# Kernel optimization log

Measured on AMD Instinct MI355X. Metric: run time of the kernel, lower is better.

The kernel has to match this reference:

```python
import jax, jax.numpy as jnp
import numpy as np
from jax import lax

B, T, V = 128, 256, 64
HF = 32   # MLP feature-imputation hidden
CTX = 32  # context hidden
HID = 64  # LSTM hidden


def _uniform(k, shape, fan):
    s = 1.0 / np.sqrt(fan)
    return jax.random.uniform(k, shape, jnp.float32, -s, s)


def setup_inputs():
    key = jax.random.key(0)
    ks = jax.random.split(key, 40)
    values = jax.random.normal(ks[0], (B, T, V), jnp.float32)
    masks = (jax.random.uniform(ks[1], (B, T, V)) > 0.3).astype(jnp.float32)
    deltas = jax.random.uniform(ks[2], (B, T, V), jnp.float32) * 5.0
    lengths = jax.random.randint(ks[3], (B,), T // 2, T + 1)
    min_vals = jnp.min(values, axis=1, keepdims=True)
    max_vals = jnp.max(values, axis=1, keepdims=True)
    D_in = 2 * V + 2 * CTX
    return dict(
        lengths=lengths, values=values, masks=masks, deltas=deltas,
        min_vals=min_vals, max_vals=max_vals,
        W_decay=_uniform(ks[4], (V, V), V), b_decay=_uniform(ks[5], (V,), V),
        W_feat=_uniform(ks[6], (V, HF, V), V), b_feat=_uniform(ks[7], (V, HF), V),
        W_nl1=_uniform(ks[8], (HF, HF), HF), b_nl1=_uniform(ks[9], (HF,), HF),
        W_nl2=_uniform(ks[10], (1, HF), HF), b_nl2=_uniform(ks[11], (1,), HF),
        Wc1=_uniform(ks[12], (2 * CTX, 3 * V + 1), 3 * V + 1), bc1=_uniform(ks[13], (2 * CTX,), 3 * V + 1),
        Wc2=_uniform(ks[14], (CTX, 2 * CTX), 2 * CTX), bc2=_uniform(ks[15], (CTX,), 2 * CTX),
        W_ih_g=_uniform(ks[16], (3 * CTX, 2 * V), CTX), W_hh_g=_uniform(ks[17], (3 * CTX, CTX), CTX),
        b_ih_g=_uniform(ks[18], (3 * CTX,), CTX), b_hh_g=_uniform(ks[19], (3 * CTX,), CTX),
        W_init=_uniform(ks[20], (2 * HID, 2 * CTX), 2 * CTX), b_init=_uniform(ks[21], (2 * HID,), 2 * CTX),
        W_ih_f=_uniform(ks[22], (4 * HID, D_in), HID), W_hh_f=_uniform(ks[23], (4 * HID, HID), HID),
        b_ih_f=_uniform(ks[24], (4 * HID,), HID), b_hh_f=_uniform(ks[25], (4 * HID,), HID),
        W_ih_b=_uniform(ks[26], (4 * HID, D_in), HID), W_hh_b=_uniform(ks[27], (4 * HID, HID), HID),
        b_ih_b=_uniform(ks[28], (4 * HID,), HID), b_hh_b=_uniform(ks[29], (4 * HID,), HID),
        W_ri=_uniform(ks[30], (V, 2 * HID), 2 * HID), b_ri=_uniform(ks[31], (V,), 2 * HID),
        W_fu=_uniform(ks[32], (V, 2 * V), 2 * V), b_fu=_uniform(ks[33], (V,), 2 * V),
    )


def _gru(x, h, Wih, Whh, bih, bhh):
    gi = x @ Wih.T + bih
    gh = h @ Whh.T + bhh
    ir, iz, inn = jnp.split(gi, 3, axis=-1)
    hr, hz, hn = jnp.split(gh, 3, axis=-1)
    r = jax.nn.sigmoid(ir + hr)
    z = jax.nn.sigmoid(iz + hz)
    n = jnp.tanh(inn + r * hn)
    return (1.0 - z) * n + z * h


def _lstm(x, h, c, Wih, Whh, bih, bhh):
    g = x @ Wih.T + bih + h @ Whh.T + bhh
    i, f, gg, o = jnp.split(g, 4, axis=-1)
    c = jax.nn.sigmoid(f) * c + jax.nn.sigmoid(i) * jnp.tanh(gg)
    h = jax.nn.sigmoid(o) * jnp.tanh(c)
    return h, c


def _forward(lengths, values, masks, deltas, min_vals, max_vals,
             W_decay, b_decay, W_feat, b_feat, W_nl1, b_nl1, W_nl2, b_nl2,
             Wc1, bc1, Wc2, bc2, W_ih_g, W_hh_g, b_ih_g, b_hh_g,
             W_init, b_init, W_ih_f, W_hh_f, b_ih_f, b_hh_f,
             W_ih_b, W_hh_b, b_ih_b, b_hh_b, W_ri, b_ri, W_fu, b_fu):
    Bb, Tt, Vv = values.shape
    lf = lengths.astype(jnp.float32)
    pad = (jnp.arange(Tt)[None, :] + 1 <= lengths[:, None]).astype(jnp.float32)  # [B,T]

    msum = masks.sum(axis=1)                       # [B,V] observation counts
    means = values.sum(axis=1) / msum
    var = ((values - means[:, None, :]) ** 2).sum(axis=1) / (msum - 1.0)
    stdev = jnp.sqrt(var)
    missing = 1.0 - msum / lf[:, None]
    stats = jnp.concatenate([lf[:, None], means, stdev, missing], axis=1)  # [B,3V+1]

    mmn = jnp.maximum(max_vals - min_vals, 1e-8)   # [B,1,V]
    nv = (values - min_vals) / mmn
    nmeans = (means - min_vals[:, 0, :]) / mmn[:, 0, :]

    # last-observation-carried-forward x_prime
    nv_tm = jnp.swapaxes(nv, 0, 1)   # [T,B,V]
    m_tm = jnp.swapaxes(masks, 0, 1)

    def pstep(xp, xm):
        x_prev, m_prev = xm
        xp = m_prev * x_prev + (1.0 - m_prev) * xp
        return xp, xp
    _, xp_rest = lax.scan(pstep, nv_tm[0], (nv_tm[:-1], m_tm[:-1]))
    x_prime = jnp.swapaxes(jnp.concatenate([nv_tm[:1], xp_rest], axis=0), 0, 1)

    # InputTemporalDecay: F.linear(d, W*I, b) == d * diag(W) + b
    gamma = jnp.exp(-jax.nn.relu(deltas * jnp.diag(W_decay) + b_decay))
    x_decay = gamma * x_prime + (1.0 - gamma) * nmeans[:, None, :]
    x_complete = masks * nv + (1.0 - masks) * x_decay

    # context vectors
    ctx_mlp = jax.nn.relu(stats @ Wc1.T + bc1) @ Wc2.T + bc2  # [B,CTX]
    x_rnn_tm = jnp.swapaxes(jnp.concatenate([x_complete, masks], axis=-1), 0, 1)  # [T,B,2V]
    pad_tm = jnp.swapaxes(pad, 0, 1)[:, :, None]
    h0 = jnp.zeros((Bb, W_hh_g.shape[1]), values.dtype)

    def gstep(carry, inp):
        h, hn = carry
        x_t, p_t = inp
        h = _gru(x_t, h, W_ih_g, W_hh_g, b_ih_g, b_hh_g)
        hn = p_t * h + (1.0 - p_t) * hn
        return (h, hn), None
    (_, ctx_rnn), _ = lax.scan(gstep, (h0, h0), (x_rnn_tm, pad_tm))
    context = jnp.concatenate([ctx_mlp, ctx_rnn], axis=1)  # [B,2*CTX]

    hinit = context @ W_init.T + b_init  # [B,2H]
    cinit = jnp.tanh(hinit)
    Hh = hinit.shape[1] // 2
    hf0, hb0 = hinit[:, :Hh], hinit[:, Hh:]
    cf0, cb0 = cinit[:, :Hh], cinit[:, Hh:]

    ctx_bt = jnp.broadcast_to(context[:, None, :], (Bb, Tt, context.shape[1]))
    rnn_in_tm = jnp.swapaxes(jnp.concatenate([x_complete, masks, ctx_bt], axis=-1), 0, 1)  # [T,B,D]

    def fstep(carry, x):
        h, c = _lstm(x, carry[0], carry[1], W_ih_f, W_hh_f, b_ih_f, b_hh_f)
        return (h, c), h
    _, hf_rest = lax.scan(fstep, (hf0, cf0), rnn_in_tm[:-1])
    hf_all = jnp.concatenate([hf0[None], hf_rest], axis=0)  # [T,B,H]

    def bstep(carry, x):
        h, c = _lstm(x, carry[0], carry[1], W_ih_b, W_hh_b, b_ih_b, b_hh_b)
        return (h, c), h
    _, hb_rest = lax.scan(bstep, (hb0, cb0), rnn_in_tm[1:][::-1])  # t = T-1 .. 1
    hb_all = jnp.concatenate([hb0[None], hb_rest], axis=0)[::-1]   # time-aligned

    h_cat = jnp.concatenate([hf_all, hb_all], axis=-1)  # [T,B,2H]
    rnn_imp = jnp.swapaxes(h_cat @ W_ri.T + b_ri, 0, 1)  # [B,T,V]

    # per-variable masked feature imputation (no self-connection)
    eye = jnp.eye(Vv, dtype=values.dtype)
    Wm = W_feat * (1.0 - eye[:, None, :])                 # [V,HF,V]
    hidden = jnp.einsum('btv,ghv->btgh', x_complete, Wm) + b_feat  # [B,T,V,HF]
    z = jax.nn.relu(hidden) @ W_nl1.T + b_nl1
    feat_imp = (jax.nn.relu(z) @ W_nl2.T + b_nl2)[..., 0]  # [B,T,V]

    beta = jax.nn.sigmoid(jnp.concatenate([gamma, masks], axis=-1) @ W_fu.T + b_fu)
    final_imp = beta * feat_imp + (1.0 - beta) * rnn_imp

    # unnormalize all three estimates; stack as [3,B,T,V]
    out = jnp.stack([rnn_imp, feat_imp, final_imp], axis=0) * mmn[None] + min_vals[None]
    return out


def reference(lengths, values, masks, deltas, min_vals, max_vals,
              W_decay, b_decay, W_feat, b_feat, W_nl1, b_nl1, W_nl2, b_nl2,
              Wc1, bc1, Wc2, bc2, W_ih_g, W_hh_g, b_ih_g, b_hh_g,
              W_init, b_init, W_ih_f, W_hh_f, b_ih_f, b_hh_f,
              W_ih_b, W_hh_b, b_ih_b, b_hh_b, W_ri, b_ri, W_fu, b_fu):
    return _forward(lengths, values, masks, deltas, min_vals, max_vals,
                    W_decay, b_decay, W_feat, b_feat, W_nl1, b_nl1, W_nl2, b_nl2,
                    Wc1, bc1, Wc2, bc2, W_ih_g, W_hh_g, b_ih_g, b_hh_g,
                    W_init, b_init, W_ih_f, W_hh_f, b_ih_f, b_hh_f,
                    W_ih_b, W_hh_b, b_ih_b, b_hh_b, W_ri, b_ri, W_fu, b_fu)
```

## Files before the change

kernel.cpp:

```cpp
#include <hip/hip_runtime.h>
#include <hip/hip_fp16.h>

static constexpr int NB = 128;
static constexpr int NT = 256;
static constexpr int NV = 64;
static constexpr int NBT = NB * NT;
static constexpr int NBTV = NBT * NV;

typedef __attribute__((ext_vector_type(8))) short short8;
typedef __attribute__((ext_vector_type(4))) float f32x4;
typedef __attribute__((ext_vector_type(4))) float fvec4;

__device__ __forceinline__ void wave_lds_fence() {
    __builtin_amdgcn_sched_barrier(0);
    asm volatile("s_waitcnt lgkmcnt(0)" ::: "memory");
    __builtin_amdgcn_sched_barrier(0);
}

__device__ __forceinline__ void block_sync_lds() {
    __builtin_amdgcn_sched_barrier(0);
    asm volatile("s_waitcnt lgkmcnt(0)" ::: "memory");
    __builtin_amdgcn_s_barrier();
    asm volatile("" ::: "memory");
    __builtin_amdgcn_sched_barrier(0);
}

__device__ __forceinline__ unsigned short f2bf(float x) {
    unsigned int u = __float_as_uint(x);
    return (unsigned short)((u + 0x7FFFu + ((u >> 16) & 1u)) >> 16);
}
__device__ __forceinline__ float bf2f(unsigned short b) {
    return __uint_as_float(((unsigned int)b) << 16);
}
__device__ __forceinline__ unsigned short f2h(float x) {
    union { _Float16 h; unsigned short u; } c; c.h = (_Float16)x; return c.u;
}
__device__ __forceinline__ float fsigm(float x) {
    return __builtin_amdgcn_rcpf(1.0f + __expf(-x));
}
__device__ __forceinline__ float ftanh(float x) {
    return 1.0f - 2.0f * __builtin_amdgcn_rcpf(1.0f + __expf(2.0f * x));
}

__device__ __forceinline__ short8 pack8(float4 a, float4 b) {
    short8 r;
    r[0] = (short)f2bf(a.x); r[1] = (short)f2bf(a.y); r[2] = (short)f2bf(a.z); r[3] = (short)f2bf(a.w);
    r[4] = (short)f2bf(b.x); r[5] = (short)f2bf(b.y); r[6] = (short)f2bf(b.z); r[7] = (short)f2bf(b.w);
    return r;
}

__device__ __forceinline__ void dot4(float4& acc, const float4 wv, const float4 xv) {
    acc.x = fmaf(wv.x, xv.x, acc.x);
    acc.y = fmaf(wv.y, xv.y, acc.y);
    acc.z = fmaf(wv.z, xv.z, acc.z);
    acc.w = fmaf(wv.w, xv.w, acc.w);
}

__global__ __launch_bounds__(256) void k_prep(
    const float* __restrict__ Wf, const float* __restrict__ Wihf,
    const float* __restrict__ Wihb, const float* __restrict__ Wihg,
    const float* __restrict__ Whhf, const float* __restrict__ Whhb,
    const float* __restrict__ Whhg, const float* __restrict__ Wri,
    const float* __restrict__ Wfu,
    unsigned short* __restrict__ wbf, float* __restrict__ wdiag,
    unsigned short* __restrict__ wgf, unsigned short* __restrict__ wgb,
    unsigned short* __restrict__ wgg,
    unsigned short* __restrict__ whhf_h, unsigned short* __restrict__ whhb_h,
    unsigned short* __restrict__ whhg_h,
    unsigned short* __restrict__ wri_bf, unsigned short* __restrict__ wfu_bf) {
    int i = blockIdx.x * 256 + threadIdx.x;
    if (i < NV * 32 * NV) wbf[i] = f2bf(Wf[i]);
    if (i < 2048) wdiag[i] = bf2f(f2bf(Wf[i * 64 + (i >> 5)]));
    if (i < 32768) {
        int n = i >> 7, k = i & 127;
        wgf[i] = f2bf(Wihf[n * 192 + k]);
        wgb[i] = f2bf(Wihb[n * 192 + k]);
    }
    if (i < 12288) wgg[i] = f2bf(Wihg[i]);
    if (i < 16384) { whhf_h[i] = f2h(Whhf[i]); whhb_h[i] = f2h(Whhb[i]); }
    if (i < 3072) whhg_h[i] = f2h(Whhg[i]);
    if (i < 8192) { wri_bf[i] = f2bf(Wri[i]); wfu_bf[i] = f2bf(Wfu[i]); }
}

__global__ __launch_bounds__(256) void k_fill(
    const int* __restrict__ lengths,
    const float* __restrict__ values, const float* __restrict__ masks,
    const float* __restrict__ deltas, const float* __restrict__ minv,
    const float* __restrict__ maxv,
    const float* __restrict__ Wd, const float* __restrict__ bd,
    float* __restrict__ stats,
    float* __restrict__ mmn_ws, float* __restrict__ nmeans_ws,
    float* __restrict__ xcomp, unsigned short* __restrict__ gam,
    const unsigned short* __restrict__ wgg, const float* __restrict__ bihg,
    float* __restrict__ gg) {
    int b = blockIdx.x; int tid = threadIdx.x;
    int v = tid & 63; int tc = tid >> 6;
    float mn = minv[b * NV + v];
    size_t base = (size_t)b * NT * NV + v;
    __shared__ float red[3][4][64];
    __shared__ float lastv[4][64];
    __shared__ int hasf[4][64];
    __shared__ float nv0s[64];
    __shared__ float smm[64], snm[64];
    __shared__ __align__(16) unsigned short sxc[256][64];
    int t0 = tc * 64;
    float sv = 0.f, sq = 0.f, sm = 0.f;
    float last = 0.f; int has = 0;
    for (int t = t0; t < t0 + 64; t++) {
        float val = values[base + (size_t)t * NV];
        float m = masks[base + (size_t)t * NV];
        sv += val; sq += val * val; sm += m;
        if (m != 0.f) { last = val; has = 1; }
        if (tc == 0 && t == 0) nv0s[v] = val;
    }
    red[0][tc][v] = sv; red[1][tc][v] = sq; red[2][tc][v] = sm;
    lastv[tc][v] = last; hasf[tc][v] = has;
    __syncthreads();
    if (tc == 0) {
        sv = red[0][0][v] + red[0][1][v] + red[0][2][v] + red[0][3][v];
        sq = red[1][0][v] + red[1][1][v] + red[1][2][v] + red[1][3][v];
        sm = red[2][0][v] + red[2][1][v] + red[2][2][v] + red[2][3][v];
        float mean = sv / sm;
        float var = (sq - 2.0f * mean * sv + (float)NT * mean * mean) / (sm - 1.0f);
        var = fmaxf(var, 0.0f);
        float sd = sqrtf(var);
        float lf = (float)lengths[b];
        float miss = 1.0f - sm / lf;
        float mx = maxv[b * NV + v];
        float mm = fmaxf(mx - mn, 1e-8f);
        float* st = stats + b * 256;
        if (v == 0) st[0] = lf;
        st[1 + v] = mean; st[65 + v] = sd; st[129 + v] = miss;
        float nmean = (mean - mn) / mm;
        mmn_ws[b * NV + v] = mm;
        nmeans_ws[b * NV + v] = nmean;
        smm[v] = mm; snm[v] = nmean;
    }
    __syncthreads();
    float mm = smm[v];
    float nmean = snm[v];
    float wd = Wd[v * NV + v], bdv = bd[v];
    float xp = (nv0s[v] - mn) / mm;
    for (int q = tc - 1; q >= 0; q--) {
        if (hasf[q][v]) { xp = (lastv[q][v] - mn) / mm; break; }
    }
    for (int t = t0; t < t0 + 64; t++) {
        size_t i = base + (size_t)t * NV;
        float val = values[i], m = masks[i], d = deltas[i];
        float nv = (val - mn) / mm;
        float g = expf(-fmaxf(fmaf(d, wd, bdv), 0.0f));
        float xd = g * xp + (1.0f - g) * nmean;
        float xc = m * nv + (1.0f - m) * xd;
        xcomp[i] = xc; gam[i] = f2bf(g);
        sxc[t][v] = f2bf(xc);
        xp = (m != 0.f) ? nv : xp;
    }
    __syncthreads();
    int lane = tid & 63;
    int r = lane & 15, kc = lane >> 4;
    for (int tile = 0; tile < 4; tile++) {
        int trow = (tc * 4 + tile) * 16;
        int bt0 = b * NT + trow;
        short8 af0 = *(const short8*)&sxc[trow + r][kc * 8];
        short8 af1 = *(const short8*)&sxc[trow + r][32 + kc * 8];
        const float* mr = masks + ((size_t)bt0 + r) * NV + kc * 8;
        short8 af2 = pack8(*(const float4*)(mr), *(const float4*)(mr + 4));
        short8 af3 = pack8(*(const float4*)(mr + 32), *(const float4*)(mr + 36));
        #pragma unroll 3
        for (int nt = 0; nt < 6; nt++) {
            const unsigned short* w = wgg + (size_t)(nt * 16 + r) * 128 + kc * 8;
            float bias = bihg[nt * 16 + r];
            f32x4 acc = {bias, bias, bias, bias};
            acc = __builtin_amdgcn_mfma_f32_16x16x32_bf16(af0, *(const short8*)(w), acc, 0, 0, 0);
            acc = __builtin_amdgcn_mfma_f32_16x16x32_bf16(af1, *(const short8*)(w + 32), acc, 0, 0, 0);
            acc = __builtin_amdgcn_mfma_f32_16x16x32_bf16(af2, *(const short8*)(w + 64), acc, 0, 0, 0);
            acc = __builtin_amdgcn_mfma_f32_16x16x32_bf16(af3, *(const short8*)(w + 96), acc, 0, 0, 0);
            #pragma unroll
            for (int i = 0; i < 4; i++)
                gg[(size_t)(bt0 + kc * 4 + i) * 96 + nt * 16 + r] = acc[i];
        }
    }
}

#define GRU_STEP(T, GIN) { \
    const int t_ = (T); const int p_ = t_ & 1; \
    int4 raw_[4]; \
    const int4* hp_ = (const int4*)hsg[g][s]; \
    _Pragma("unroll") for (int q = 0; q < 4; q++) raw_[q] = hp_[q]; \
    const __half2* hhv_ = (const __half2*)raw_; \
    __half2 a0_ = zh2, a1_ = zh2, a2_ = zh2, a3_ = zh2; \
    _Pragma("unroll") for (int q = 0; q < 16; q += 4) { \
        a0_ = __hfma2(w2[q],     hhv_[q],     a0_); \
        a1_ = __hfma2(w2[q + 1], hhv_[q + 1], a1_); \
        a2_ = __hfma2(w2[q + 2], hhv_[q + 2], a2_); \
        a3_ = __hfma2(w2[q + 3], hhv_[q + 3], a3_); } \
    __half2 sA_ = __hadd2(__hadd2(a0_, a1_), __hadd2(a2_, a3_)); \
    float d_ = __low2float(sA_) + __high2float(sA_); \
    if (g < 2) { \
        gexg[p_][s][n][g] = GIN + bh + d_; \
    } else { \
        gexg[p_][s][n][2] = bh + d_; \
        gexg[p_][s][n][3] = GIN; \
    } \
    block_sync_lds(); \
    float qx_ = gexg[p_][s][n][0], qy_ = gexg[p_][s][n][1]; \
    float qz_ = gexg[p_][s][n][2], qw_ = gexg[p_][s][n][3]; \
    float rr_ = fsigm(qx_); \
    float zz_ = fsigm(qy_); \
    float nn_ = ftanh(qw_ + rr_ * qz_); \
    float h_ = (1.f - zz_) * nn_ + zz_ * hprev; \
    hprev = h_; \
    if (t_ < len) hn = h_; \
    hsg[g][s][n] = f2h(h_); \
    wave_lds_fence(); \
}

#define FEAT_BODY(BT0) { \
    int bt0 = (BT0); \
    int r = lane & 15, kc = lane >> 4; \
    unsigned short* hbw = hbs[wave]; \
    float* lx = ldsx[wave]; \
    float* flw = fls[wave]; \
    short8 a0, a1; \
    { \
        const float* xr = xcomp + (size_t)(bt0 + r) * NV + kc * 8; \
        a0 = pack8(*(const float4*)(xr), *(const float4*)(xr + 4)); \
        a1 = pack8(*(const float4*)(xr + 32), *(const float4*)(xr + 36)); \
    } \
    { \
        int gc0 = kc * 16; \
        const float* xr2 = xcomp + (size_t)(bt0 + r) * NV + gc0; \
        _Pragma("unroll") for (int e = 0; e < 16; e += 4) { \
            float4 p = *(const float4*)(xr2 + e); \
            lx[(gc0 + e + 0) * 16 + r] = bf2f(f2bf(p.x)); \
            lx[(gc0 + e + 1) * 16 + r] = bf2f(f2bf(p.y)); \
            lx[(gc0 + e + 2) * 16 + r] = bf2f(f2bf(p.z)); \
            lx[(gc0 + e + 3) * 16 + r] = bf2f(f2bf(p.w)); \
        } \
    } \
    short8 wb0, wb1; \
    { \
        const float* w = Wnl1 + r * 32 + kc * 8; \
        wb0 = pack8(*(const float4*)w, *(const float4*)(w + 4)); \
        const float* w2p = Wnl1 + (16 + r) * 32 + kc * 8; \
        wb1 = pack8(*(const float4*)w2p, *(const float4*)(w2p + 4)); \
    } \
    float b0i[4], b1i[4], w2a[4], w2b[4]; \
    _Pragma("unroll") for (int i = 0; i < 4; i++) { \
        b0i[i] = bnl1[kc * 4 + i]; \
        b1i[i] = bnl1[16 + kc * 4 + i]; \
        w2a[i] = Wnl2[kc * 4 + i]; \
        w2b[i] = Wnl2[16 + kc * 4 + i]; \
    } \
    float bn2 = bnl2[0]; \
    __builtin_amdgcn_wave_barrier(); \
    _Pragma("unroll 2") for (int g = 0; g < 64; g++) { \
        __builtin_amdgcn_wave_barrier(); \
        float xv[4]; \
        _Pragma("unroll") for (int i = 0; i < 4; i++) xv[i] = lx[g * 16 + kc * 4 + i]; \
        _Pragma("unroll") for (int f = 0; f < 2; f++) { \
            int n0 = g * 32 + f * 16; \
            const unsigned short* wrow = wbf + (size_t)(n0 + r) * 64; \
            short8 b0 = *(const short8*)(wrow + kc * 8); \
            short8 b1 = *(const short8*)(wrow + 32 + kc * 8); \
            f32x4 acc = {0.f, 0.f, 0.f, 0.f}; \
            acc = __builtin_amdgcn_mfma_f32_16x16x32_bf16(a0, b0, acc, 0, 0, 0); \
            acc = __builtin_amdgcn_mfma_f32_16x16x32_bf16(a1, b1, acc, 0, 0, 0); \
            int n = n0 + r; \
            float wd = wdiag[n], bs = bfeat[n]; \
            _Pragma("unroll") for (int i = 0; i < 4; i++) { \
                float h = acc[i] - xv[i] * wd + bs; \
                h = fmaxf(h, 0.0f); \
                hbw[(kc * 4 + i) * 32 + f * 16 + r] = f2bf(h); \
            } \
        } \
        __builtin_amdgcn_wave_barrier(); \
        short8 ah = *(const short8*)(hbw + r * 32 + kc * 8); \
        f32x4 zt0 = {0.f, 0.f, 0.f, 0.f}, zt1 = {0.f, 0.f, 0.f, 0.f}; \
        zt0 = __builtin_amdgcn_mfma_f32_16x16x32_bf16(wb0, ah, zt0, 0, 0, 0); \
        zt1 = __builtin_amdgcn_mfma_f32_16x16x32_bf16(wb1, ah, zt1, 0, 0, 0); \
        float p = 0.f; \
        _Pragma("unroll") for (int i = 0; i < 4; i++) { \
            p = fmaf(fmaxf(zt0[i] + b0i[i], 0.0f), w2a[i], p); \
            p = fmaf(fmaxf(zt1[i] + b1i[i], 0.0f), w2b[i], p); \
        } \
        p += __shfl_xor(p, 16, 64); \
        p += __shfl_xor(p, 32, 64); \
        if (lane < 16) flw[lane * 65 + g] = p + bn2; \
    } \
    __builtin_amdgcn_wave_barrier(); \
    _Pragma("unroll") for (int q = 0; q < 16; q++) \
        feat_out[(size_t)(bt0 + q) * NV + lane] = flw[q * 65 + lane]; \
}

__global__ __launch_bounds__(256, 1) void k_mid(
    const float* __restrict__ gg_t, const int* __restrict__ lengths,
    const unsigned short* __restrict__ whhg_h, const float* __restrict__ bhh,
    float* __restrict__ ctx,
    const float* __restrict__ stats, const float* __restrict__ Wc1,
    const float* __restrict__ bc1, const float* __restrict__ Wc2,
    const float* __restrict__ bc2,
    const float* __restrict__ xcomp, const float* __restrict__ masks,
    const unsigned short* __restrict__ wbf,
    const float* __restrict__ wdiag, const float* __restrict__ bfeat,
    const float* __restrict__ Wnl1, const float* __restrict__ bnl1,
    const float* __restrict__ Wnl2, const float* __restrict__ bnl2,
    float* __restrict__ feat_out,
    const unsigned short* __restrict__ wgf, const unsigned short* __restrict__ wgb,
    float* __restrict__ gf, float* __restrict__ gb) {
    __shared__ __align__(16) unsigned short hsg[3][2][32];
    __shared__ __align__(16) float gexg[2][2][32][5];
    __shared__ __align__(16) float ss[193];
    __shared__ float h1[64];
    __shared__ __align__(16) unsigned short hbs[4][16 * 32];
    __shared__ __align__(16) float ldsx[4][64 * 16];
    __shared__ __align__(16) float fls[4][16 * 65];

    int bx = blockIdx.x;
    int tid = threadIdx.x;

    if (bx < 64) {
        int b0 = bx * 2;
        int g = tid >> 6;
        int lane = tid & 63;
        int s = lane >> 5, n = lane & 31;
        if (g == 3) {
            for (int t = 0; t < NT; t++) block_sync_lds();
            return;
        }
        int b = b0 + s;
        const __half2 zh2 = __float2half2_rn(0.f);
        int4 w4[4];
        {
            const int4* wp = (const int4*)(whhg_h + (size_t)(g * 32 + n) * 32);
            #pragma unroll
            for (int q = 0; q < 4; q++) w4[q] = wp[q];
        }
        const __half2* w2 = (const __half2*)w4;
        float bh = bhh[g * 32 + n];
        int len = lengths[b];
        float hprev = 0.f, hn = 0.f;
        hsg[g][s][n] = f2h(0.f);
        const float* gbase = gg_t + (size_t)b * NT * 96;
        #define GGIDX(T) ((size_t)(T) * 96 + g * 32 + n)
        float gi0 = gbase[GGIDX(0)];
        float gi1 = gbase[GGIDX(1)];
        float gi2 = gbase[GGIDX(2)];
        float gi3 = gbase[GGIDX(3)];
        wave_lds_fence();
        for (int t = 0; t < 252; t += 4) {
            GRU_STEP(t, gi0)
            gi0 = gbase[GGIDX(t + 4)];
            GRU_STEP(t + 1, gi1)
            gi1 = gbase[GGIDX(t + 5)];
            GRU_STEP(t + 2, gi2)
            gi2 = gbase[GGIDX(t + 6)];
            GRU_STEP(t + 3, gi3)
            gi3 = gbase[GGIDX(t + 7)];
        }
        GRU_STEP(252, gi0)
        GRU_STEP(253, gi1)
        GRU_STEP(254, gi2)
        GRU_STEP(255, gi3)
        #undef GGIDX
        if (g == 0) ctx[(b0 + s) * 64 + 32 + n] = hn;
    } else if (bx < 192) {
        if (tid >= 64) return;
        int b = bx - 64;
        ss[tid] = stats[b * 256 + tid];
        ss[64 + tid] = stats[b * 256 + 64 + tid];
        ss[128 + tid] = stats[b * 256 + 128 + tid];
        if (tid == 0) ss[192] = stats[b * 256 + 192];
        wave_lds_fence();
        float acc = bc1[tid];
        const float* w = Wc1 + (size_t)tid * 193;
        for (int k = 0; k < 193; k++) acc = fmaf(w[k], ss[k], acc);
        h1[tid] = fmaxf(acc, 0.f);
        wave_lds_fence();
        if (tid < 32) {
            float a = bc2[tid];
            const float* w2 = Wc2 + tid * 64;
            for (int k = 0; k < 64; k++) a = fmaf(w2[k], h1[k], a);
            ctx[b * 64 + tid] = a;
        }
    } else if (bx < 448) {
        int wave = tid >> 6; int lane = tid & 63;
        FEAT_BODY((bx - 192) * 64 + wave * 16)
    } else {
        int wave = tid >> 6, lane = tid & 63;
        int bt0 = (bx - 448) * 64 + wave * 16;
        int r = lane & 15, kc = lane >> 4;
        const float* xr = xcomp + (size_t)(bt0 + r) * NV + kc * 8;
        const float* mr = masks + (size_t)(bt0 + r) * NV + kc * 8;
        short8 af0 = pack8(*(const float4*)(xr), *(const float4*)(xr + 4));
        short8 af1 = pack8(*(const float4*)(xr + 32), *(const float4*)(xr + 36));
        short8 af2 = pack8(*(const float4*)(mr), *(const float4*)(mr + 4));
        short8 af3 = pack8(*(const float4*)(mr + 32), *(const float4*)(mr + 36));
        #pragma unroll 4
        for (int nt = 0; nt < 16; nt++) {
            const unsigned short* w = wgf + (size_t)(nt * 16 + r) * 128 + kc * 8;
            f32x4 acc = {0.f, 0.f, 0.f, 0.f};
            acc = __builtin_amdgcn_mfma_f32_16x16x32_bf16(af0, *(const short8*)(w), acc, 0, 0, 0);
            acc = __builtin_amdgcn_mfma_f32_16x16x32_bf16(af1, *(const short8*)(w + 32), acc, 0, 0, 0);
            acc = __builtin_amdgcn_mfma_f32_16x16x32_bf16(af2, *(const short8*)(w + 64), acc, 0, 0, 0);
            acc = __builtin_amdgcn_mfma_f32_16x16x32_bf16(af3, *(const short8*)(w + 96), acc, 0, 0, 0);
            int col = nt * 16 + r, g = col >> 6, n = col & 63;
            #pragma unroll
            for (int i = 0; i < 4; i++)
                gf[((size_t)(bt0 + kc * 4 + i) * 64 + n) * 4 + g] = acc[i];
        }
        #pragma unroll 4
        for (int nt = 0; nt < 16; nt++) {
            const unsigned short* w = wgb + (size_t)(nt * 16 + r) * 128 + kc * 8;
            f32x4 acc = {0.f, 0.f, 0.f, 0.f};
            acc = __builtin_amdgcn_mfma_f32_16x16x32_bf16(af0, *(const short8*)(w), acc, 0, 0, 0);
            acc = __builtin_amdgcn_mfma_f32_16x16x32_bf16(af1, *(const short8*)(w + 32), acc, 0, 0, 0);
            acc = __builtin_amdgcn_mfma_f32_16x16x32_bf16(af2, *(const short8*)(w + 64), acc, 0, 0, 0);
            acc = __builtin_amdgcn_mfma_f32_16x16x32_bf16(af3, *(const short8*)(w + 96), acc, 0, 0, 0);
            int col = nt * 16 + r, g = col >> 6, n = col & 63;
            #pragma unroll
            for (int i = 0; i < 4; i++)
                gb[((size_t)(bt0 + kc * 4 + i) * 64 + n) * 4 + g] = acc[i];
        }
    }
}

#define LSTM_STEP(S, GIN) { \
    const int s_ = (S); const int p_ = s_ & 1; \
    int4 raw_[8]; \
    const int4* hp_ = (const int4*)hs[g]; \
    _Pragma("unroll") for (int q = 0; q < 8; q++) raw_[q] = hp_[q]; \
    const __half2* hhv_ = (const __half2*)raw_; \
    __half2 a0_ = zh2, a1_ = zh2, a2_ = zh2, a3_ = zh2; \
    _Pragma("unroll") for (int q = 0; q < 32; q += 4) { \
        a0_ = __hfma2(w2[q],     hhv_[q],     a0_); \
        a1_ = __hfma2(w2[q + 1], hhv_[q + 1], a1_); \
        a2_ = __hfma2(w2[q + 2], hhv_[q + 2], a2_); \
        a3_ = __hfma2(w2[q + 3], hhv_[q + 3], a3_); } \
    __half2 sA_ = __hadd2(__hadd2(a0_, a1_), __hadd2(a2_, a3_)); \
    float d_ = __low2float(sA_) + __high2float(sA_); \
    gex[p_][n][g] = GIN + ctg + d_; \
    block_sync_lds(); \
    float qx_ = gex[p_][n][0], qy_ = gex[p_][n][1]; \
    float qz_ = gex[p_][n][2], qw_ = gex[p_][n][3]; \
    float ii_ = fsigm(qx_); \
    float ff_ = fsigm(qy_); \
    float gv_ = ftanh(qz_); \
    float oo_ = fsigm(qw_); \
    c = ff_ * c + ii_ * gv_; \
    float hv_ = oo_ * ftanh(c); \
    if (g == 0) { \
        int tout_ = dir ? (NT - 2 - s_) : (s_ + 1); \
        hall[((size_t)b * NT + tout_) * NV + n] = hv_; \
    } \
    hs[g][n] = f2h(hv_); \
    wave_lds_fence(); \
}

__global__ __launch_bounds__(256, 1) void k_lstm(
    const float* __restrict__ gf, const float* __restrict__ gb,
    const float* __restrict__ ctx,
    const unsigned short* __restrict__ whhf_h, const unsigned short* __restrict__ whhb_h,
    const float* __restrict__ Wihf, const float* __restrict__ Wihb,
    const float* __restrict__ bihf, const float* __restrict__ bhhf,
    const float* __restrict__ bihb, const float* __restrict__ bhhb,
    const float* __restrict__ Wini, const float* __restrict__ bini,
    float* __restrict__ out0, float* __restrict__ out1,
    const float* __restrict__ xcomp, const unsigned short* __restrict__ wbf,
    const float* __restrict__ wdiag, const float* __restrict__ bfeat,
    const float* __restrict__ Wnl1, const float* __restrict__ bnl1,
    const float* __restrict__ Wnl2, const float* __restrict__ bnl2,
    float* __restrict__ feat_out) {
    __shared__ __align__(16) unsigned short hs[4][64];
    __shared__ __align__(16) float gex[2][64][5];
    __shared__ __align__(16) float sctx[64];
    __shared__ __align__(16) float sh0[64];
    __shared__ __align__(16) unsigned short hbs[4][16 * 32];
    __shared__ __align__(16) float ldsx[4][64 * 16];
    __shared__ __align__(16) float fls[4][16 * 65];

    int bx = blockIdx.x;
    int tid = threadIdx.x;

    if (bx >= 256) {
        int wave = tid >> 6; int lane = tid & 63;
        FEAT_BODY((bx - 256) * 64 + 16384 + wave * 16)
        return;
    }

    int dir = bx >> 7; int b = bx & 127;
    int g = tid >> 6;
    int n = tid & 63;
    const float* gates = dir ? gb : gf;
    const unsigned short* wsrc = dir ? whhb_h : whhf_h;
    float* hall = dir ? out1 : out0;
    const __half2 zh2 = __float2half2_rn(0.f);
    int4 w4[8];
    {
        const int4* wp = (const int4*)(wsrc + (size_t)(g * 64 + n) * 64);
        #pragma unroll
        for (int q = 0; q < 8; q++) w4[q] = wp[q];
    }
    const __half2* w2 = (const __half2*)w4;
    size_t gbase = (size_t)b * NT * 256;
    #define GIDX(S) (gbase + (size_t)(dir ? (NT - 1 - (S)) : (S)) * 256 + n * 4 + g)
    float gi0 = gates[GIDX(0)];
    float gi1 = gates[GIDX(1)];
    float gi2 = gates[GIDX(2)];
    float gi3 = gates[GIDX(3)];
    if (tid < 64) sctx[tid] = ctx[b * 64 + tid];
    __syncthreads();
    float ctg;
    {
        const float4* wc = (const float4*)((dir ? Wihb : Wihf) + (size_t)tid * 192 + 128);
        float bias = dir ? (bihb[tid] + bhhb[tid]) : (bihf[tid] + bhhf[tid]);
        const float4* c4 = (const float4*)sctx;
        float4 a = {0, 0, 0, 0};
        #pragma unroll
        for (int q = 0; q < 16; q++) dot4(a, wc[q], c4[q]);
        ctg = bias + a.x + a.y + a.z + a.w;
    }
    if (tid < 64) {
        const float4* wi = (const float4*)(Wini + (size_t)(dir * 64 + tid) * 64);
        const float4* c4 = (const float4*)sctx;
        float4 a = {0, 0, 0, 0};
        #pragma unroll
        for (int q = 0; q < 16; q++) dot4(a, wi[q], c4[q]);
        sh0[tid] = bini[dir * 64 + tid] + a.x + a.y + a.z + a.w;
    }
    __syncthreads();
    float c;
    {
        float h0 = sh0[n];
        c = ftanh(h0);
        hs[g][n] = f2h(h0);
        if (g == 0) {
            int t0 = dir ? (NT - 1) : 0;
            hall[((size_t)b * NT + t0) * NV + n] = h0;
        }
    }
    wave_lds_fence();
    for (int sx = 0; sx < 252; sx += 4) {
        LSTM_STEP(sx, gi0)
        gi0 = gates[GIDX(sx + 4)];
        LSTM_STEP(sx + 1, gi1)
        gi1 = gates[GIDX(sx + 5)];
        LSTM_STEP(sx + 2, gi2)
        gi2 = gates[GIDX(sx + 6)];
        LSTM_STEP(sx + 3, gi3)
        gi3 = gates[GIDX(sx + 7)];
    }
    LSTM_STEP(252, gi0)
    LSTM_STEP(253, gi1)
    LSTM_STEP(254, gi2)
    #undef GIDX
}

__global__ __launch_bounds__(256) void k_post(
    const unsigned short* __restrict__ gam, const float* __restrict__ masks,
    const unsigned short* __restrict__ wri_bf, const unsigned short* __restrict__ wfu_bf,
    const float* __restrict__ bri, const float* __restrict__ bfu,
    const float* __restrict__ mmn_ws, const float* __restrict__ minv,
    float* out0, float* out1, float* out2) {
    int wave = threadIdx.x >> 6, lane = threadIdx.x & 63;
    int bt0 = blockIdx.x * 64 + wave * 16;
    int r = lane & 15, kc = lane >> 4;
    int b = bt0 >> 8;
    const float* h0r = out0 + (size_t)(bt0 + r) * NV + kc * 8;
    const float* h1r = out1 + (size_t)(bt0 + r) * NV + kc * 8;
    const unsigned short* gr = gam + (size_t)(bt0 + r) * NV + kc * 8;
    const float* mr  = masks + (size_t)(bt0 + r) * NV + kc * 8;
    short8 A0 = pack8(*(const float4*)(h0r), *(const float4*)(h0r + 4));
    short8 A1 = pack8(*(const float4*)(h0r + 32), *(const float4*)(h0r + 36));
    short8 A2 = pack8(*(const float4*)(h1r), *(const float4*)(h1r + 4));
    short8 A3 = pack8(*(const float4*)(h1r + 32), *(const float4*)(h1r + 36));
    short8 G0 = *(const short8*)(gr);
    short8 G1 = *(const short8*)(gr + 32);
    short8 M0 = pack8(*(const float4*)(mr), *(const float4*)(mr + 4));
    short8 M1 = pack8(*(const float4*)(mr + 32), *(const float4*)(mr + 36));
    #pragma unroll
    for (int nt = 0; nt < 4; nt++) {
        int n = nt * 16 + r;
        const unsigned short* wr = wri_bf + (size_t)n * 128 + kc * 8;
        const unsigned short* wf = wfu_bf + (size_t)n * 128 + kc * 8;
        float bi = bri[n], bf_ = bfu[n];
        f32x4 racc = {bi, bi, bi, bi};
        f32x4 bacc = {bf_, bf_, bf_, bf_};
        racc = __builtin_amdgcn_mfma_f32_16x16x32_bf16(A0, *(const short8*)(wr), racc, 0, 0, 0);
        racc = __builtin_amdgcn_mfma_f32_16x16x32_bf16(A1, *(const short8*)(wr + 32), racc, 0, 0, 0);
        racc = __builtin_amdgcn_mfma_f32_16x16x32_bf16(A2, *(const short8*)(wr + 64), racc, 0, 0, 0);
        racc = __builtin_amdgcn_mfma_f32_16x16x32_bf16(A3, *(const short8*)(wr + 96), racc, 0, 0, 0);
        bacc = __builtin_amdgcn_mfma_f32_16x16x32_bf16(G0, *(const short8*)(wf), bacc, 0, 0, 0);
        bacc = __builtin_amdgcn_mfma_f32_16x16x32_bf16(G1, *(const short8*)(wf + 32), bacc, 0, 0, 0);
        bacc = __builtin_amdgcn_mfma_f32_16x16x32_bf16(M0, *(const short8*)(wf + 64), bacc, 0, 0, 0);
        bacc = __builtin_amdgcn_mfma_f32_16x16x32_bf16(M1, *(const short8*)(wf + 96), bacc, 0, 0, 0);
        float mm = mmn_ws[b * NV + n], mn = minv[b * NV + n];
        #pragma unroll
        for (int i = 0; i < 4; i++) {
            int row = bt0 + kc * 4 + i;
            size_t idx = (size_t)row * NV + n;
            float rn = racc[i];
            float beta = fsigm(bacc[i]);
            float ft = out2[idx];
            float fin = beta * ft + (1.0f - beta) * rn;
            out0[idx] = fmaf(rn, mm, mn);
            out1[idx] = fmaf(ft, mm, mn);
            out2[idx] = fmaf(fin, mm, mn);
        }
    }
}

extern "C" void kernel_launch(void* const* d_in, const int* in_sizes, int n_in,
                              void* d_out, int out_size, void* d_ws, size_t ws_size,
                              hipStream_t stream) {
    const int*   lengths  = (const int*)d_in[0];
    const float* values   = (const float*)d_in[1];
    const float* masks    = (const float*)d_in[2];
    const float* deltas   = (const float*)d_in[3];
    const float* min_vals = (const float*)d_in[4];
    const float* max_vals = (const float*)d_in[5];
    const float* W_decay  = (const float*)d_in[6];
    const float* b_decay  = (const float*)d_in[7];
    const float* W_feat   = (const float*)d_in[8];
    const float* b_feat   = (const float*)d_in[9];
    const float* W_nl1    = (const float*)d_in[10];
    const float* b_nl1    = (const float*)d_in[11];
    const float* W_nl2    = (const float*)d_in[12];
    const float* b_nl2    = (const float*)d_in[13];
    const float* Wc1      = (const float*)d_in[14];
    const float* bc1      = (const float*)d_in[15];
    const float* Wc2      = (const float*)d_in[16];
    const float* bc2      = (const float*)d_in[17];
    const float* W_ih_g   = (const float*)d_in[18];
    const float* W_hh_g   = (const float*)d_in[19];
    const float* b_ih_g   = (const float*)d_in[20];
    const float* b_hh_g   = (const float*)d_in[21];
    const float* W_init   = (const float*)d_in[22];
    const float* b_init   = (const float*)d_in[23];
    const float* W_ih_f   = (const float*)d_in[24];
    const float* W_hh_f   = (const float*)d_in[25];
    const float* b_ih_f   = (const float*)d_in[26];
    const float* b_hh_f   = (const float*)d_in[27];
    const float* W_ih_b   = (const float*)d_in[28];
    const float* W_hh_b   = (const float*)d_in[29];
    const float* b_ih_b   = (const float*)d_in[30];
    const float* b_hh_b   = (const float*)d_in[31];
    const float* W_ri     = (const float*)d_in[32];
    const float* b_ri     = (const float*)d_in[33];
    const float* W_fu     = (const float*)d_in[34];
    const float* b_fu     = (const float*)d_in[35];

    float* ws = (float*)d_ws;
    float* xcomp  = ws;
    unsigned short* gam = (unsigned short*)(ws + 2097152);
    unsigned short* wri_bf = (unsigned short*)(ws + 4194304);
    unsigned short* wfu_bf = (unsigned short*)(ws + 4198400);
    float* stats  = ws + 6291456;
    float* mmn    = ws + 6324224;
    float* nmeans = ws + 6332416;
    float* ctx    = ws + 6340608;
    unsigned short* wbf = (unsigned short*)(ws + 6365184);
    float* wdiag  = ws + 6430720;
    unsigned short* wgf = (unsigned short*)(ws + 6432768);
    unsigned short* wgb = (unsigned short*)(ws + 6449152);
    unsigned short* wgg = (unsigned short*)(ws + 6465536);
    unsigned short* whhf_h = (unsigned short*)(ws + 6471680);
    unsigned short* whhb_h = (unsigned short*)(ws + 6479872);
    unsigned short* whhg_h = (unsigned short*)(ws + 6488064);
    float* gates_f = ws + 6555136;
    float* gates_b = ws + 14943744;
    float* gates_g = ws + 23332352;

    float* out0 = (float*)d_out;
    float* out1 = out0 + NBTV;
    float* out2 = out0 + 2 * NBTV;

    k_prep<<<512, 256, 0, stream>>>(W_feat, W_ih_f, W_ih_b, W_ih_g, W_hh_f, W_hh_b, W_hh_g,
                                    W_ri, W_fu,
                                    wbf, wdiag, wgf, wgb, wgg, whhf_h, whhb_h, whhg_h,
                                    wri_bf, wfu_bf);
    k_fill<<<NB, 256, 0, stream>>>(lengths, values, masks, deltas, min_vals, max_vals,
                                   W_decay, b_decay, stats, mmn, nmeans, xcomp, gam,
                                   wgg, b_ih_g, gates_g);
    k_mid<<<960, 256, 0, stream>>>(gates_g, lengths, whhg_h, b_hh_g, ctx,
                                   stats, Wc1, bc1, Wc2, bc2,
                                   xcomp, masks, wbf, wdiag, b_feat, W_nl1, b_nl1, W_nl2, b_nl2, out2,
                                   wgf, wgb, gates_f, gates_b);
    k_lstm<<<512, 256, 0, stream>>>(gates_f, gates_b, ctx, whhf_h, whhb_h,
                                    W_ih_f, W_ih_b, b_ih_f, b_hh_f, b_ih_b, b_hh_b,
                                    W_init, b_init, out0, out1,
                                    xcomp, wbf, wdiag, b_feat, W_nl1, b_nl1, W_nl2, b_nl2, out2);
    k_post<<<NBT / 64, 256, 0, stream>>>(gam, masks, wri_bf, wfu_bf, b_ri, b_fu, mmn, min_vals,
                                         out0, out1, out2);
}
```

Before: 270.7 us.

## Compute all three GRU gates per lane to remove block barriers

The context GRU recurrence used to spread the three gates over three waves, which exchanged partial sums through LDS with a block barrier at every timestep. Now each lane computes the r, z and n dot products itself and keeps all three hidden-weight rows in registers, so a step needs only a wave-local LDS fence. Each wave handles two sequences independently, which packs the GRU into 16 blocks instead of 64, and the gate input buffer is interleaved so each lane reads r, z and n from adjacent addresses. In exchange each lane does three times the FMA work per step and holds more registers.

```diff
diff --git a/kernel.cpp b/kernel.cpp
--- a/kernel.cpp
+++ b/kernel.cpp
@@ -175,17 +175,18 @@
             acc = __builtin_amdgcn_mfma_f32_16x16x32_bf16(af1, *(const short8*)(w + 32), acc, 0, 0, 0);
             acc = __builtin_amdgcn_mfma_f32_16x16x32_bf16(af2, *(const short8*)(w + 64), acc, 0, 0, 0);
             acc = __builtin_amdgcn_mfma_f32_16x16x32_bf16(af3, *(const short8*)(w + 96), acc, 0, 0, 0);
+            int col = nt * 16 + r;
+            int gx = col >> 5, nn2 = col & 31;
             #pragma unroll
             for (int i = 0; i < 4; i++)
-                gg[(size_t)(bt0 + kc * 4 + i) * 96 + nt * 16 + r] = acc[i];
+                gg[(size_t)(bt0 + kc * 4 + i) * 96 + nn2 * 3 + gx] = acc[i];
         }
     }
 }
 
-#define GRU_STEP(T, GIN) { \
-    const int t_ = (T); const int p_ = t_ & 1; \
+#define GRU_STEP(T, GR, GZ, GN) { \
     int4 raw_[4]; \
-    const int4* hp_ = (const int4*)hsg[g][s]; \
+    const int4* hp_ = (const int4*)hsg[wid][s]; \
     _Pragma("unroll") for (int q = 0; q < 4; q++) raw_[q] = hp_[q]; \
     const __half2* hhv_ = (const __half2*)raw_; \
     __half2 a0_ = zh2, a1_ = zh2, a2_ = zh2, a3_ = zh2; \
@@ -195,23 +196,30 @@
         a2_ = __hfma2(w2[q + 2], hhv_[q + 2], a2_); \
         a3_ = __hfma2(w2[q + 3], hhv_[q + 3], a3_); } \
     __half2 sA_ = __hadd2(__hadd2(a0_, a1_), __hadd2(a2_, a3_)); \
-    float d_ = __low2float(sA_) + __high2float(sA_); \
-    if (g < 2) { \
-        gexg[p_][s][n][g] = GIN + bh + d_; \
-    } else { \
-        gexg[p_][s][n][2] = bh + d_; \
-        gexg[p_][s][n][3] = GIN; \
-    } \
-    block_sync_lds(); \
-    float qx_ = gexg[p_][s][n][0], qy_ = gexg[p_][s][n][1]; \
-    float qz_ = gexg[p_][s][n][2], qw_ = gexg[p_][s][n][3]; \
-    float rr_ = fsigm(qx_); \
-    float zz_ = fsigm(qy_); \
-    float nn_ = ftanh(qw_ + rr_ * qz_); \
+    float dr_ = __low2float(sA_) + __high2float(sA_); \
+    a0_ = zh2; a1_ = zh2; a2_ = zh2; a3_ = zh2; \
+    _Pragma("unroll") for (int q = 0; q < 16; q += 4) { \
+        a0_ = __hfma2(w2[16 + q],     hhv_[q],     a0_); \
+        a1_ = __hfma2(w2[16 + q + 1], hhv_[q + 1], a1_); \
+        a2_ = __hfma2(w2[16 + q + 2], hhv_[q + 2], a2_); \
+        a3_ = __hfma2(w2[16 + q + 3], hhv_[q + 3], a3_); } \
+    sA_ = __hadd2(__hadd2(a0_, a1_), __hadd2(a2_, a3_)); \
+    float dz_ = __low2float(sA_) + __high2float(sA_); \
+    a0_ = zh2; a1_ = zh2; a2_ = zh2; a3_ = zh2; \
+    _Pragma("unroll") for (int q = 0; q < 16; q += 4) { \
+        a0_ = __hfma2(w2[32 + q],     hhv_[q],     a0_); \
+        a1_ = __hfma2(w2[32 + q + 1], hhv_[q + 1], a1_); \
+        a2_ = __hfma2(w2[32 + q + 2], hhv_[q + 2], a2_); \
+        a3_ = __hfma2(w2[32 + q + 3], hhv_[q + 3], a3_); } \
+    sA_ = __hadd2(__hadd2(a0_, a1_), __hadd2(a2_, a3_)); \
+    float dn_ = __low2float(sA_) + __high2float(sA_); \
+    float rr_ = fsigm((GR) + bh0 + dr_); \
+    float zz_ = fsigm((GZ) + bh1 + dz_); \
+    float nn_ = ftanh((GN) + rr_ * (bh2 + dn_)); \
     float h_ = (1.f - zz_) * nn_ + zz_ * hprev; \
     hprev = h_; \
-    if (t_ < len) hn = h_; \
-    hsg[g][s][n] = f2h(h_); \
+    if ((T) < len) hn = h_; \
+    hsg[wid][s][n] = f2h(h_); \
     wave_lds_fence(); \
 }
 
@@ -308,8 +316,7 @@
     float* __restrict__ feat_out,
     const unsigned short* __restrict__ wgf, const unsigned short* __restrict__ wgb,
     float* __restrict__ gf, float* __restrict__ gb) {
-    __shared__ __align__(16) unsigned short hsg[3][2][32];
-    __shared__ __align__(16) float gexg[2][2][32][5];
+    __shared__ __align__(16) unsigned short hsg[4][2][32];
     __shared__ __align__(16) float ss[193];
     __shared__ float h1[64];
     __shared__ __align__(16) unsigned short hbs[4][16 * 32];
@@ -319,54 +326,52 @@
     int bx = blockIdx.x;
     int tid = threadIdx.x;
 
-    if (bx < 64) {
-        int b0 = bx * 2;
-        int g = tid >> 6;
+    if (bx < 16) {
+        int wid = tid >> 6;
         int lane = tid & 63;
         int s = lane >> 5, n = lane & 31;
-        if (g == 3) {
-            for (int t = 0; t < NT; t++) block_sync_lds();
-            return;
-        }
-        int b = b0 + s;
+        int b = bx * 8 + wid * 2 + s;
         const __half2 zh2 = __float2half2_rn(0.f);
-        int4 w4[4];
+        int4 w4[12];
         {
-            const int4* wp = (const int4*)(whhg_h + (size_t)(g * 32 + n) * 32);
             #pragma unroll
-            for (int q = 0; q < 4; q++) w4[q] = wp[q];
+            for (int g = 0; g < 3; g++) {
+                const int4* wp = (const int4*)(whhg_h + (size_t)(g * 32 + n) * 32);
+                #pragma unroll
+                for (int q = 0; q < 4; q++) w4[g * 4 + q] = wp[q];
+            }
         }
         const __half2* w2 = (const __half2*)w4;
-        float bh = bhh[g * 32 + n];
+        float bh0 = bhh[n], bh1 = bhh[32 + n], bh2 = bhh[64 + n];
         int len = lengths[b];
         float hprev = 0.f, hn = 0.f;
-        hsg[g][s][n] = f2h(0.f);
-        const float* gbase = gg_t + (size_t)b * NT * 96;
-        #define GGIDX(T) ((size_t)(T) * 96 + g * 32 + n)
-        float gi0 = gbase[GGIDX(0)];
-        float gi1 = gbase[GGIDX(1)];
-        float gi2 = gbase[GGIDX(2)];
-        float gi3 = gbase[GGIDX(3)];
+        hsg[wid][s][n] = f2h(0.f);
+        const float* gbase = gg_t + (size_t)b * NT * 96 + n * 3;
+        #define GGP(T) (gbase + (size_t)(T) * 96)
+        float gr0 = GGP(0)[0], gz0 = GGP(0)[1], gn0 = GGP(0)[2];
+        float gr1 = GGP(1)[0], gz1 = GGP(1)[1], gn1 = GGP(1)[2];
+        float gr2 = GGP(2)[0], gz2 = GGP(2)[1], gn2 = GGP(2)[2];
+        float gr3 = GGP(3)[0], gz3 = GGP(3)[1], gn3 = GGP(3)[2];
         wave_lds_fence();
         for (int t = 0; t < 252; t += 4) {
-            GRU_STEP(t, gi0)
-            gi0 = gbase[GGIDX(t + 4)];
-            GRU_STEP(t + 1, gi1)
-            gi1 = gbase[GGIDX(t + 5)];
-            GRU_STEP(t + 2, gi2)
-            gi2 = gbase[GGIDX(t + 6)];
-            GRU_STEP(t + 3, gi3)
-            gi3 = gbase[GGIDX(t + 7)];
+            GRU_STEP(t, gr0, gz0, gn0)
+            { const float* p = GGP(t + 4); gr0 = p[0]; gz0 = p[1]; gn0 = p[2]; }
+            GRU_STEP(t + 1, gr1, gz1, gn1)
+            { const float* p = GGP(t + 5); gr1 = p[0]; gz1 = p[1]; gn1 = p[2]; }
+            GRU_STEP(t + 2, gr2, gz2, gn2)
+            { const float* p = GGP(t + 6); gr2 = p[0]; gz2 = p[1]; gn2 = p[2]; }
+            GRU_STEP(t + 3, gr3, gz3, gn3)
+            { const float* p = GGP(t + 7); gr3 = p[0]; gz3 = p[1]; gn3 = p[2]; }
         }
-        GRU_STEP(252, gi0)
-        GRU_STEP(253, gi1)
-        GRU_STEP(254, gi2)
-        GRU_STEP(255, gi3)
-        #undef GGIDX
-        if (g == 0) ctx[(b0 + s) * 64 + 32 + n] = hn;
-    } else if (bx < 192) {
+        GRU_STEP(252, gr0, gz0, gn0)
+        GRU_STEP(253, gr1, gz1, gn1)
+        GRU_STEP(254, gr2, gz2, gn2)
+        GRU_STEP(255, gr3, gz3, gn3)
+        #undef GGP
+        ctx[b * 64 + 32 + n] = hn;
+    } else if (bx < 144) {
         if (tid >= 64) return;
-        int b = bx - 64;
+        int b = bx - 16;
         ss[tid] = stats[b * 256 + tid];
         ss[64 + tid] = stats[b * 256 + 64 + tid];
         ss[128 + tid] = stats[b * 256 + 128 + tid];
@@ -383,12 +388,12 @@
             for (int k = 0; k < 64; k++) a = fmaf(w2[k], h1[k], a);
             ctx[b * 64 + tid] = a;
         }
-    } else if (bx < 448) {
+    } else if (bx < 400) {
         int wave = tid >> 6; int lane = tid & 63;
-        FEAT_BODY((bx - 192) * 64 + wave * 16)
+        FEAT_BODY((bx - 144) * 64 + wave * 16)
     } else {
         int wave = tid >> 6, lane = tid & 63;
-        int bt0 = (bx - 448) * 64 + wave * 16;
+        int bt0 = (bx - 400) * 64 + wave * 16;
         int r = lane & 15, kc = lane >> 4;
         const float* xr = xcomp + (size_t)(bt0 + r) * NV + kc * 8;
         const float* mr = masks + (size_t)(bt0 + r) * NV + kc * 8;
@@ -682,7 +687,7 @@
     k_fill<<<NB, 256, 0, stream>>>(lengths, values, masks, deltas, min_vals, max_vals,
                                    W_decay, b_decay, stats, mmn, nmeans, xcomp, gam,
                                    wgg, b_ih_g, gates_g);
-    k_mid<<<960, 256, 0, stream>>>(gates_g, lengths, whhg_h, b_hh_g, ctx,
+    k_mid<<<912, 256, 0, stream>>>(gates_g, lengths, whhg_h, b_hh_g, ctx,
                                    stats, Wc1, bc1, Wc2, bc2,
                                    xcomp, masks, wbf, wdiag, b_feat, W_nl1, b_nl1, W_nl2, b_nl2, out2,
                                    wgf, wgb, gates_f, gates_b);
```

Measured after the change: 273.5 us. Within noise of the previous version (+1.0%).

## Map each LSTM sequence to one wave, removing per-step block barriers

Applied to the files above, without the earlier changes.

Each LSTM recurrence (batch × direction) now runs in a single wavefront instead of a 256-thread block. Each lane computes all four gates for its hidden unit, holding 4x more recurrent weights in registers and loading gate inputs as float4. This removes the per-step LDS exchange and block-wide barrier, leaving only a wave-local LDS fence per step. In exchange each lane does 4x the FMA work per step, and register pressure rises; the grid shrinks to 64 LSTM blocks plus the feature blocks.

```diff
diff --git a/kernel.cpp b/kernel.cpp
--- a/kernel.cpp
+++ b/kernel.cpp
@@ -425,35 +425,31 @@
     }
 }
 
-#define LSTM_STEP(S, GIN) { \
-    const int s_ = (S); const int p_ = s_ & 1; \
+#define LSTM_STEP2(S, GI) { \
     int4 raw_[8]; \
-    const int4* hp_ = (const int4*)hs[g]; \
+    const int4* hp_ = (const int4*)hsw[wid]; \
     _Pragma("unroll") for (int q = 0; q < 8; q++) raw_[q] = hp_[q]; \
     const __half2* hhv_ = (const __half2*)raw_; \
-    __half2 a0_ = zh2, a1_ = zh2, a2_ = zh2, a3_ = zh2; \
-    _Pragma("unroll") for (int q = 0; q < 32; q += 4) { \
-        a0_ = __hfma2(w2[q],     hhv_[q],     a0_); \
-        a1_ = __hfma2(w2[q + 1], hhv_[q + 1], a1_); \
-        a2_ = __hfma2(w2[q + 2], hhv_[q + 2], a2_); \
-        a3_ = __hfma2(w2[q + 3], hhv_[q + 3], a3_); } \
-    __half2 sA_ = __hadd2(__hadd2(a0_, a1_), __hadd2(a2_, a3_)); \
-    float d_ = __low2float(sA_) + __high2float(sA_); \
-    gex[p_][n][g] = GIN + ctg + d_; \
-    block_sync_lds(); \
-    float qx_ = gex[p_][n][0], qy_ = gex[p_][n][1]; \
-    float qz_ = gex[p_][n][2], qw_ = gex[p_][n][3]; \
-    float ii_ = fsigm(qx_); \
-    float ff_ = fsigm(qy_); \
-    float gv_ = ftanh(qz_); \
-    float oo_ = fsigm(qw_); \
+    float dd_[4]; \
+    _Pragma("unroll") for (int g = 0; g < 4; g++) { \
+        __half2 a0_ = zh2, a1_ = zh2, a2_ = zh2, a3_ = zh2; \
+        _Pragma("unroll") for (int q = 0; q < 32; q += 4) { \
+            a0_ = __hfma2(w2[g * 32 + q],     hhv_[q],     a0_); \
+            a1_ = __hfma2(w2[g * 32 + q + 1], hhv_[q + 1], a1_); \
+            a2_ = __hfma2(w2[g * 32 + q + 2], hhv_[q + 2], a2_); \
+            a3_ = __hfma2(w2[g * 32 + q + 3], hhv_[q + 3], a3_); } \
+        __half2 sA_ = __hadd2(__hadd2(a0_, a1_), __hadd2(a2_, a3_)); \
+        dd_[g] = __low2float(sA_) + __high2float(sA_); \
+    } \
+    float ii_ = fsigm(GI.x + ctg0 + dd_[0]); \
+    float ff_ = fsigm(GI.y + ctg1 + dd_[1]); \
+    float gv_ = ftanh(GI.z + ctg2 + dd_[2]); \
+    float oo_ = fsigm(GI.w + ctg3 + dd_[3]); \
     c = ff_ * c + ii_ * gv_; \
     float hv_ = oo_ * ftanh(c); \
-    if (g == 0) { \
-        int tout_ = dir ? (NT - 2 - s_) : (s_ + 1); \
-        hall[((size_t)b * NT + tout_) * NV + n] = hv_; \
-    } \
-    hs[g][n] = f2h(hv_); \
+    int tout_ = dir ? (NT - 2 - (S)) : ((S) + 1); \
+    hall[((size_t)b * NT + tout_) * NV + n] = hv_; \
+    hsw[wid][n] = f2h(hv_); \
     wave_lds_fence(); \
 }
 
@@ -471,10 +467,8 @@
     const float* __restrict__ Wnl1, const float* __restrict__ bnl1,
     const float* __restrict__ Wnl2, const float* __restrict__ bnl2,
     float* __restrict__ feat_out) {
-    __shared__ __align__(16) unsigned short hs[4][64];
-    __shared__ __align__(16) float gex[2][64][5];
-    __shared__ __align__(16) float sctx[64];
-    __shared__ __align__(16) float sh0[64];
+    __shared__ __align__(16) unsigned short hsw[4][64];
+    __shared__ __align__(16) float sctxw[4][64];
     __shared__ __align__(16) unsigned short hbs[4][16 * 32];
     __shared__ __align__(16) float ldsx[4][64 * 16];
     __shared__ __align__(16) float fls[4][16 * 65];
@@ -482,78 +476,86 @@
     int bx = blockIdx.x;
     int tid = threadIdx.x;
 
-    if (bx >= 256) {
+    if (bx >= 64) {
         int wave = tid >> 6; int lane = tid & 63;
-        FEAT_BODY((bx - 256) * 64 + 16384 + wave * 16)
+        FEAT_BODY((bx - 64) * 64 + 16384 + wave * 16)
         return;
     }
 
-    int dir = bx >> 7; int b = bx & 127;
-    int g = tid >> 6;
+    int wid = tid >> 6;
     int n = tid & 63;
+    int rid = bx * 4 + wid;
+    int dir = rid >> 7; int b = rid & 127;
     const float* gates = dir ? gb : gf;
     const unsigned short* wsrc = dir ? whhb_h : whhf_h;
     float* hall = dir ? out1 : out0;
     const __half2 zh2 = __float2half2_rn(0.f);
-    int4 w4[8];
-    {
+    int4 w4[32];
+    #pragma unroll
+    for (int g = 0; g < 4; g++) {
         const int4* wp = (const int4*)(wsrc + (size_t)(g * 64 + n) * 64);
         #pragma unroll
-        for (int q = 0; q < 8; q++) w4[q] = wp[q];
+        for (int q = 0; q < 8; q++) w4[g * 8 + q] = wp[q];
     }
     const __half2* w2 = (const __half2*)w4;
-    size_t gbase = (size_t)b * NT * 256;
-    #define GIDX(S) (gbase + (size_t)(dir ? (NT - 1 - (S)) : (S)) * 256 + n * 4 + g)
-    float gi0 = gates[GIDX(0)];
-    float gi1 = gates[GIDX(1)];
-    float gi2 = gates[GIDX(2)];
-    float gi3 = gates[GIDX(3)];
-    if (tid < 64) sctx[tid] = ctx[b * 64 + tid];
-    __syncthreads();
-    float ctg;
+    sctxw[wid][n] = ctx[b * 64 + n];
+    wave_lds_fence();
+    float ctg0, ctg1, ctg2, ctg3;
     {
-        const float4* wc = (const float4*)((dir ? Wihb : Wihf) + (size_t)tid * 192 + 128);
-        float bias = dir ? (bihb[tid] + bhhb[tid]) : (bihf[tid] + bhhf[tid]);
-        const float4* c4 = (const float4*)sctx;
-        float4 a = {0, 0, 0, 0};
+        const float* base_ih = dir ? Wihb : Wihf;
+        const float4* c4 = (const float4*)sctxw[wid];
+        const float4* wc0 = (const float4*)(base_ih + (size_t)(0 * 64 + n) * 192 + 128);
+        const float4* wc1 = (const float4*)(base_ih + (size_t)(1 * 64 + n) * 192 + 128);
+        const float4* wc2 = (const float4*)(base_ih + (size_t)(2 * 64 + n) * 192 + 128);
+        const float4* wc3 = (const float4*)(base_ih + (size_t)(3 * 64 + n) * 192 + 128);
+        float4 a0 = {0,0,0,0}, a1 = {0,0,0,0}, a2 = {0,0,0,0}, a3 = {0,0,0,0};
         #pragma unroll
-        for (int q = 0; q < 16; q++) dot4(a, wc[q], c4[q]);
-        ctg = bias + a.x + a.y + a.z + a.w;
-    }
-    if (tid < 64) {
-        const float4* wi = (const float4*)(Wini + (size_t)(dir * 64 + tid) * 64);
-        const float4* c4 = (const float4*)sctx;
+        for (int q = 0; q < 16; q++) {
+            float4 cv = c4[q];
+            dot4(a0, wc0[q], cv); dot4(a1, wc1[q], cv);
+            dot4(a2, wc2[q], cv); dot4(a3, wc3[q], cv);
+        }
+        const float* bih = dir ? bihb : bihf;
+        const float* bhh2 = dir ? bhhb : bhhf;
+        ctg0 = bih[n]       + bhh2[n]       + a0.x + a0.y + a0.z + a0.w;
+        ctg1 = bih[64 + n]  + bhh2[64 + n]  + a1.x + a1.y + a1.z + a1.w;
+        ctg2 = bih[128 + n] + bhh2[128 + n] + a2.x + a2.y + a2.z + a2.w;
+        ctg3 = bih[192 + n] + bhh2[192 + n] + a3.x + a3.y + a3.z + a3.w;
+    }
+    float c;
+    {
+        const float4* wi = (const float4*)(Wini + (size_t)(dir * 64 + n) * 64);
+        const float4* c4 = (const float4*)sctxw[wid];
         float4 a = {0, 0, 0, 0};
         #pragma unroll
         for (int q = 0; q < 16; q++) dot4(a, wi[q], c4[q]);
-        sh0[tid] = bini[dir * 64 + tid] + a.x + a.y + a.z + a.w;
-    }
-    __syncthreads();
-    float c;
-    {
-        float h0 = sh0[n];
+        float h0 = bini[dir * 64 + n] + a.x + a.y + a.z + a.w;
         c = ftanh(h0);
-        hs[g][n] = f2h(h0);
-        if (g == 0) {
-            int t0 = dir ? (NT - 1) : 0;
-            hall[((size_t)b * NT + t0) * NV + n] = h0;
-        }
+        hsw[wid][n] = f2h(h0);
+        int t0 = dir ? (NT - 1) : 0;
+        hall[((size_t)b * NT + t0) * NV + n] = h0;
     }
     wave_lds_fence();
+    size_t gbase = (size_t)b * NT * 256 + (size_t)n * 4;
+    #define GP(S) (*(const float4*)(gates + gbase + (size_t)(dir ? (NT - 1 - (S)) : (S)) * 256))
+    float4 gi0 = GP(0);
+    float4 gi1 = GP(1);
+    float4 gi2 = GP(2);
+    float4 gi3 = GP(3);
     for (int sx = 0; sx < 252; sx += 4) {
-        LSTM_STEP(sx, gi0)
-        gi0 = gates[GIDX(sx + 4)];
-        LSTM_STEP(sx + 1, gi1)
-        gi1 = gates[GIDX(sx + 5)];
-        LSTM_STEP(sx + 2, gi2)
-        gi2 = gates[GIDX(sx + 6)];
-        LSTM_STEP(sx + 3, gi3)
-        gi3 = gates[GIDX(sx + 7)];
-    }
-    LSTM_STEP(252, gi0)
-    LSTM_STEP(253, gi1)
-    LSTM_STEP(254, gi2)
-    #undef GIDX
+        LSTM_STEP2(sx, gi0)
+        gi0 = GP(sx + 4);
+        LSTM_STEP2(sx + 1, gi1)
+        gi1 = GP(sx + 5);
+        LSTM_STEP2(sx + 2, gi2)
+        gi2 = GP(sx + 6);
+        LSTM_STEP2(sx + 3, gi3)
+        gi3 = GP(sx + 7);
+    }
+    LSTM_STEP2(252, gi0)
+    LSTM_STEP2(253, gi1)
+    LSTM_STEP2(254, gi2)
+    #undef GP
 }
 
 __global__ __launch_bounds__(256) void k_post(
@@ -686,7 +688,7 @@
                                    stats, Wc1, bc1, Wc2, bc2,
                                    xcomp, masks, wbf, wdiag, b_feat, W_nl1, b_nl1, W_nl2, b_nl2, out2,
                                    wgf, wgb, gates_f, gates_b);
-    k_lstm<<<512, 256, 0, stream>>>(gates_f, gates_b, ctx, whhf_h, whhb_h,
+    k_lstm<<<320, 256, 0, stream>>>(gates_f, gates_b, ctx, whhf_h, whhb_h,
                                     W_ih_f, W_ih_b, b_ih_f, b_hh_f, b_ih_b, b_hh_b,
                                     W_init, b_init, out0, out1,
                                     xcomp, wbf, wdiag, b_feat, W_nl1, b_nl1, W_nl2, b_nl2, out2);
```

Measured after the change: 298.9 us. 1.1x slower.
